# Kernel tuning notes

Hardware: AMD Instinct MI355X
Metric: run time of the kernel (lower is better)

Reference implementation:

```python
import math
import jax, jax.numpy as jnp
import numpy as np

N = 262144
DIMS_IN = 8
DIMS_C = 4
UNITS = 64
BINS = 10
N_PERMS = 3  # ceil(log2(8))
N_BLOCKS = 2 * N_PERMS
MIN_BW = 0.001
MIN_BH = 0.001
MIN_D = 0.001
EPS = 1e-6
LOG2 = float(np.log(2.0))


def build_masks():
    bits = np.array([[int(ch) for ch in np.binary_repr(i, N_PERMS)] for i in range(DIMS_IN)])
    bits = bits[:, ::-1].T  # (N_PERMS, DIMS_IN), LSB-first
    m = np.repeat(bits, 2, axis=0).astype(bool)  # repeat_interleave(2, dim=0)
    m[1::2] ^= True
    return m

MASKS = build_masks()  # (6, 8) bool, each row has 4 True


def rational_quadratic_spline(inputs, uw, uh, ud):
    # inputs: (N, D); uw/uh: (N, D, K); ud: (N, D, K+1). left=bottom=0, right=top=1.
    K = uw.shape[-1]
    widths = MIN_BW + (1.0 - MIN_BW * K) * jax.nn.softmax(uw, axis=-1)
    cw = jnp.cumsum(widths, axis=-1)
    cw = jnp.concatenate([jnp.zeros_like(cw[..., :1]), cw], axis=-1)
    cw = cw.at[..., -1].set(1.0)
    widths = cw[..., 1:] - cw[..., :-1]

    deriv = (MIN_D + jax.nn.softplus(ud)) / (MIN_D + LOG2)

    heights = MIN_BH + (1.0 - MIN_BH * K) * jax.nn.softmax(uh, axis=-1)
    ch = jnp.cumsum(heights, axis=-1)
    ch = jnp.concatenate([jnp.zeros_like(ch[..., :1]), ch], axis=-1)
    ch = ch.at[..., -1].set(1.0)
    heights = ch[..., 1:] - ch[..., :-1]

    # searchsorted on bin edges (forward uses cumwidths)
    locs = cw.at[..., -1].add(EPS)
    bin_idx = jnp.clip(jnp.sum(inputs[..., None] >= locs, axis=-1) - 1, 0, K - 1)
    g = lambda a: jnp.take_along_axis(a, bin_idx[..., None], axis=-1)[..., 0]

    in_cw = g(cw)
    in_bw = g(widths)
    in_ch = g(ch)
    delta = heights / widths
    in_delta = g(delta)
    in_d = g(deriv)
    in_dp1 = g(deriv[..., 1:])
    in_h = g(heights)

    theta = (inputs - in_cw) / in_bw
    tomt = theta * (1.0 - theta)
    numerator = in_h * (in_delta * theta ** 2 + in_d * tomt)
    denominator = in_delta + (in_d + in_dp1 - 2.0 * in_delta) * tomt
    outputs = in_ch + numerator / denominator
    deriv_num = in_delta ** 2 * (in_dp1 * theta ** 2 + 2.0 * in_delta * tomt + in_d * (1.0 - theta) ** 2)
    logabsdet = jnp.log(deriv_num) - 2.0 * jnp.log(denominator)
    return outputs, logabsdet


def unconstrained_rqs(inputs, uw, uh, ud):
    inside = jnp.all((inputs >= 0.0) & (inputs <= 1.0), axis=-1)  # (N,)
    x_in = jnp.clip(inputs, 0.0, 1.0)
    o, lad = rational_quadratic_spline(x_in, uw, uh, ud)
    outputs = jnp.where(inside[:, None], o, inputs)
    logabsdet = jnp.where(inside[:, None], lad, 0.0)
    return outputs, logabsdet


def setup_inputs() -> dict:
    key = jax.random.key(0)
    ks = jax.random.split(key, 10)
    out_dim = 4 * (3 * BINS + 1)  # every mask has 4 transformed dims
    in_dim = 4 + DIMS_C
    inp = {
        'x': jax.random.uniform(ks[0], (N, DIMS_IN), dtype=jnp.float32),
        'c': jax.random.normal(ks[1], (N, DIMS_C), dtype=jnp.float32),
        'W1': jax.random.normal(ks[2], (N_BLOCKS, in_dim, UNITS), dtype=jnp.float32) * 0.1,
        'b1': jax.random.normal(ks[3], (N_BLOCKS, UNITS), dtype=jnp.float32) * 0.1,
        'W2': jax.random.normal(ks[4], (N_BLOCKS, UNITS, UNITS), dtype=jnp.float32) * 0.1,
        'b2': jax.random.normal(ks[5], (N_BLOCKS, UNITS), dtype=jnp.float32) * 0.1,
        'W3': jax.random.normal(ks[6], (N_BLOCKS, UNITS, out_dim), dtype=jnp.float32) * 0.1,
        'b3': jax.random.normal(ks[7], (N_BLOCKS, out_dim), dtype=jnp.float32) * 0.1,
    }
    return inp


def reference(x, c, W1, b1, W2, b2, W3, b3):
    # ConditionalFlow.log_prob: forward transform, returns jac
    jac = jnp.zeros((x.shape[0],), dtype=x.dtype)
    for i in range(N_BLOCKS):
        mask = MASKS[i]
        cond_idx = np.nonzero(mask)[0]
        trafo_idx = np.nonzero(~mask)[0]
        x_cond = jnp.concatenate([x[:, cond_idx], c], axis=1)
        h = jax.nn.leaky_relu(x_cond @ W1[i] + b1[i], 0.01)
        h = jax.nn.leaky_relu(h @ W2[i] + b2[i], 0.01)
        out = (h @ W3[i] + b3[i]).reshape(x.shape[0], len(trafo_idx), 3 * BINS + 1)
        x_t = x[:, trafo_idx]
        x_out, bj = unconstrained_rqs(x_t, out[..., :BINS], out[..., BINS:2 * BINS], out[..., 2 * BINS:])
        x = x.at[:, trafo_idx].set(x_out)
        jac = jac + bj.sum(axis=1)
    return jac
```

## Files before the change

### kernel.cpp

```cpp
#include <hip/hip_runtime.h>
#include <hip/hip_bf16.h>
#include <math.h>

#define TPB 1024
#define NWV 16
#define WGS 256
#define NBLK 6
#define DNORM (1.0f / (0.001f + 0.69314718055994530942f))

typedef float  f32x4  __attribute__((ext_vector_type(4)));
typedef short  bf16x8 __attribute__((ext_vector_type(8)));

#define MFMA16(A, B, C) __builtin_amdgcn_mfma_f32_16x16x32_bf16((A), (B), (C), 0, 0, 0)


__device__ __forceinline__ float leaky(float a) { return a >= 0.f ? a : 0.01f * a; }

__device__ __forceinline__ unsigned int bfbits(float f) {
    unsigned int u = __float_as_uint(f);
    return (u + 0x7fffu + ((u >> 16) & 1u)) >> 16;
}

__device__ __forceinline__ unsigned int pkcvt(float a, float b) {
    __hip_bfloat162 t = __float22bfloat162_rn(make_float2(a, b));
    union { __hip_bfloat162 b2; unsigned int u; } cv;
    cv.b2 = t;
    return cv.u;
}

__global__ void prep_kernel(const float* __restrict__ W1, const float* __restrict__ B1,
                            const float* __restrict__ W2, const float* __restrict__ B2,
                            const float* __restrict__ W3, const float* __restrict__ B3,
                            unsigned short* __restrict__ wsf)
{
    const int blk = blockIdx.x;
    const int tid = threadIdx.x;
    unsigned short* baseA = wsf + blk * 1024;
    unsigned short* baseB = wsf + 6144 + blk * 12288;
    const float* w1 = W1 + blk * 512;
    const float* w2 = W2 + blk * 4096;
    const float* w3 = W3 + blk * 7936;

    if (tid < 512) {
        const int tile = tid >> 7, u = (tid >> 3) & 15, i = tid & 7;
        baseA[tid] = (unsigned short)bfbits(w1[i * 64 + tile * 16 + u]);
    }
    float* bb = reinterpret_cast<float*>(baseA + 512);
    if (tid >= 512 && tid < 576)        bb[tid - 512]      = B1[blk * 64 + (tid - 512)];
    else if (tid >= 576 && tid < 640)   bb[tid - 512]      = B2[blk * 64 + (tid - 576)];
    else if (tid >= 640 && tid < 768) {
        const int j = tid - 640;
        bb[128 + j] = (j < 124) ? B3[blk * 124 + j] : 0.f;
    }

    for (int e = tid; e < 4096; e += 1024) {
        const int ks = e >> 11, tile = (e >> 9) & 3, lane = (e >> 3) & 63, i = e & 7;
        const int k = ks * 32 + (lane >> 4) * 8 + i, col = tile * 16 + (lane & 15);
        baseB[e] = (unsigned short)bfbits(w2[k * 64 + col]);
    }
    for (int e = tid; e < 8192; e += 1024) {
        const int ks = e >> 12, tile = (e >> 9) & 7, lane = (e >> 3) & 63, i = e & 7;
        const int k = ks * 32 + (lane >> 4) * 8 + i, col = tile * 16 + (lane & 15);
        const float f = (col < 124) ? w3[k * 124 + col] : 0.f;
        baseB[4096 + e] = (unsigned short)bfbits(f);
    }
}

__global__ __launch_bounds__(TPB, 4) void flow_kernel(
    const float* __restrict__ X, const float* __restrict__ C4,
    const unsigned short* __restrict__ WSF, float* __restrict__ JAC)
{
    __shared__ __align__(16) unsigned short s_w[6144];
    __shared__ __align__(16) unsigned char  s_u[126976];
    __shared__ __align__(16) float          s_x[2304];

    const int tid   = threadIdx.x;
    const int wv    = tid >> 6;
    const int ln    = tid & 63;
    const int col16 = ln & 15;
    const int g     = ln >> 4;
    const int srow  = wv * 16 + col16;
    const int wgBase = blockIdx.x * WGS;

    unsigned short* hh = reinterpret_cast<unsigned short*>(s_u + wv * 7936);
    float*          op = reinterpret_cast<float*>(s_u + wv * 7936);

    {
        const int s  = tid >> 2;
        const int d0 = (tid & 3) * 2;
        const float2 xv = reinterpret_cast<const float2*>(X)[(size_t)(wgBase + s) * 4 + (tid & 3)];
        s_x[s * 9 + d0]     = xv.x;
        s_x[s * 9 + d0 + 1] = xv.y;
    }
    const float4 cvv = reinterpret_cast<const float4*>(C4)[(size_t)wgBase + srow];

    if (wv < 12) {
        const int off = wv * 512;
        __builtin_amdgcn_global_load_lds(
            (const __attribute__((address_space(1))) unsigned int*)(WSF + off + ln * 8),
            (__attribute__((address_space(3))) unsigned int*)(&s_w[off]),
            16, 0, 0);
    }
    __syncthreads();

    const int fB = g * 4;
    float jacl = 0.f;

    #pragma unroll 1
    for (int blk = 0; blk < NBLK; ++blk) {
        const int wA = blk * 1024;
        const float* biasf = reinterpret_cast<const float*>(&s_w[wA + 512]);
        const unsigned short* wBg = WSF + 6144 + blk * 12288;

        const int p  = blk >> 1;
        const int cb = (blk & 1) ^ 1;
        const int tb = blk & 1;
        const int lm = (1 << p) - 1;

        float xcf[8];
        #pragma unroll
        for (int j = 0; j < 4; ++j) {
            const int cd = ((j >> p) << (p + 1)) | (cb << p) | (j & lm);
            xcf[j] = s_x[srow * 9 + cd];
        }
        xcf[4] = cvv.x; xcf[5] = cvv.y; xcf[6] = cvv.z; xcf[7] = cvv.w;

        union { unsigned int u[4]; bf16x8 v; } bxh;
        #pragma unroll
        for (int q = 0; q < 4; ++q)
            bxh.u[q] = (g == 0) ? pkcvt(xcf[2 * q], xcf[2 * q + 1]) : 0u;

        #pragma unroll
        for (int tile = 0; tile < 4; ++tile) {
            f32x4 a1 = *reinterpret_cast<const f32x4*>(&biasf[tile * 16 + fB]);
            const bf16x8 wh = *reinterpret_cast<const bf16x8*>(&s_w[wA + tile * 128 + col16 * 8]);
            a1 = MFMA16(wh, bxh.v, a1);
            uint2 pw;
            pw.x = pkcvt(leaky(a1[0]), leaky(a1[1]));
            pw.y = pkcvt(leaky(a1[2]), leaky(a1[3]));
            *reinterpret_cast<uint2*>(&hh[col16 * 72 + tile * 16 + fB]) = pw;
        }

        f32x4 acc2[4];
        #pragma unroll
        for (int tile = 0; tile < 4; ++tile)
            acc2[tile] = *reinterpret_cast<const f32x4*>(&biasf[64 + tile * 16 + fB]);
        #pragma unroll
        for (int ks = 0; ks < 2; ++ks) {
            const bf16x8 hf = *reinterpret_cast<const bf16x8*>(&hh[col16 * 72 + ks * 32 + g * 8]);
            #pragma unroll
            for (int tile = 0; tile < 4; ++tile) {
                const bf16x8 wh = *reinterpret_cast<const bf16x8*>(
                    wBg + (ks * 4 + tile) * 512 + ln * 8);
                acc2[tile] = MFMA16(wh, hf, acc2[tile]);
            }
        }
        #pragma unroll
        for (int tile = 0; tile < 4; ++tile) {
            uint2 pw;
            pw.x = pkcvt(leaky(acc2[tile][0]), leaky(acc2[tile][1]));
            pw.y = pkcvt(leaky(acc2[tile][2]), leaky(acc2[tile][3]));
            *reinterpret_cast<uint2*>(&hh[col16 * 72 + tile * 16 + fB]) = pw;
        }

        f32x4 acc3[8];
        #pragma unroll
        for (int tile = 0; tile < 8; ++tile)
            acc3[tile] = *reinterpret_cast<const f32x4*>(&biasf[128 + tile * 16 + fB]);
        #pragma unroll
        for (int ks = 0; ks < 2; ++ks) {
            const bf16x8 hf = *reinterpret_cast<const bf16x8*>(&hh[col16 * 72 + ks * 32 + g * 8]);
            #pragma unroll
            for (int tile = 0; tile < 8; ++tile) {
                const bf16x8 wh = *reinterpret_cast<const bf16x8*>(
                    wBg + 4096 + (ks * 8 + tile) * 512 + ln * 8);
                acc3[tile] = MFMA16(wh, hf, acc3[tile]);
            }
        }

        #pragma unroll
        for (int tile = 0; tile < 8; ++tile)
            if (tile * 16 + fB < 124)
                *reinterpret_cast<f32x4*>(&op[col16 * 124 + tile * 16 + fB]) = acc3[tile];

        float xt[4];
        #pragma unroll
        for (int j = 0; j < 4; ++j) {
            const int td = ((j >> p) << (p + 1)) | (tb << p) | (j & lm);
            xt[j] = s_x[srow * 9 + td];
        }
        const float xmn = fminf(fminf(xt[0], xt[1]), fminf(xt[2], xt[3]));
        const float xmx = fmaxf(fmaxf(xt[0], xt[1]), fmaxf(xt[2], xt[3]));
        const bool inside = (xmn >= 0.f) && (xmx <= 1.f);
        float xtv = (g == 1) ? xt[1] : xt[0];
        xtv = (g == 2) ? xt[2] : xtv;
        xtv = (g == 3) ? xt[3] : xtv;
        const int ti = ((g >> p) << (p + 1)) | (tb << p) | (g & lm);

        float ov[31];
        {
            const float* ob = op + col16 * 124 + g * 31;
            #pragma unroll
            for (int j = 0; j < 31; ++j) ov[j] = ob[j];
        }

        float ew[10];
        #pragma unroll
        for (int k = 0; k < 10; ++k) ew[k] = __expf(ov[k]);
        const float sw = (((ew[0] + ew[1]) + (ew[2] + ew[3])) + ((ew[4] + ew[5]) + (ew[6] + ew[7])))
                         + (ew[8] + ew[9]);
        const float fw = 0.99f / sw;
        float Cw[11];
        Cw[0] = 0.f;
        #pragma unroll
        for (int k = 1; k <= 9; ++k) Cw[k] = Cw[k - 1] + (0.001f + ew[k - 1] * fw);
        Cw[10] = 1.0f;

        float eh[10];
        #pragma unroll
        for (int k = 0; k < 10; ++k) eh[k] = __expf(ov[10 + k]);
        const float sh = (((eh[0] + eh[1]) + (eh[2] + eh[3])) + ((eh[4] + eh[5]) + (eh[6] + eh[7])))
                         + (eh[8] + eh[9]);
        const float fh = 0.99f / sh;
        float Ch[11];
        Ch[0] = 0.f;
        #pragma unroll
        for (int k = 1; k <= 9; ++k) Ch[k] = Ch[k - 1] + (0.001f + eh[k - 1] * fh);
        Ch[10] = 1.0f;

        const float xin = fminf(fmaxf(xtv, 0.f), 1.f);
        float in_cw = 0.f, in_cwp1 = Cw[1], in_ch = 0.f, in_chp1 = Ch[1];
        float u_d = ov[20], u_dp1 = ov[21];
        #pragma unroll
        for (int k = 1; k < 10; ++k) {
            const bool ge = (xin >= Cw[k]);
            in_cw   = ge ? Cw[k]      : in_cw;
            in_cwp1 = ge ? Cw[k + 1]  : in_cwp1;
            in_ch   = ge ? Ch[k]      : in_ch;
            in_chp1 = ge ? Ch[k + 1]  : in_chp1;
            u_d     = ge ? ov[20 + k] : u_d;
            u_dp1   = ge ? ov[21 + k] : u_dp1;
        }
        const float in_bw = in_cwp1 - in_cw;
        const float in_h  = in_chp1 - in_ch;
        const float sp_d   = (u_d   > 15.f) ? u_d   : __logf(1.f + __expf(u_d));
        const float sp_dp1 = (u_dp1 > 15.f) ? u_dp1 : __logf(1.f + __expf(u_dp1));
        const float in_d   = (0.001f + sp_d)   * DNORM;
        const float in_dp1 = (0.001f + sp_dp1) * DNORM;

        const float th   = (xin - in_cw) / in_bw;
        const float tomt = th * (1.f - th);
        const float dl   = in_h / in_bw;
        const float nume = in_h * (dl * th * th + in_d * tomt);
        const float deno = dl + (in_d + in_dp1 - 2.f * dl) * tomt;
        const float xout = in_ch + nume / deno;
        const float omt  = 1.f - th;
        const float dnum = dl * dl * (in_dp1 * th * th + 2.f * dl * tomt + in_d * omt * omt);
        const float lad  = __logf(dnum) - 2.f * __logf(deno);

        jacl += inside ? lad : 0.f;
        s_x[srow * 9 + ti] = inside ? xout : xtv;
    }

    jacl += __shfl_xor(jacl, 16);
    jacl += __shfl_xor(jacl, 32);
    if (ln < 16)
        JAC[(size_t)wgBase + wv * 16 + ln] = jacl;
}

extern "C" void kernel_launch(void* const* d_in, const int* in_sizes, int n_in,
                              void* d_out, int out_size, void* d_ws, size_t ws_size,
                              hipStream_t stream) {
    (void)n_in; (void)ws_size;
    const float* X  = (const float*)d_in[0];
    const float* C4 = (const float*)d_in[1];
    const float* W1 = (const float*)d_in[2];
    const float* B1 = (const float*)d_in[3];
    const float* W2 = (const float*)d_in[4];
    const float* B2 = (const float*)d_in[5];
    const float* W3 = (const float*)d_in[6];
    const float* B3 = (const float*)d_in[7];
    float* out = (float*)d_out;
    unsigned short* wsf = (unsigned short*)d_ws;

    hipLaunchKernelGGL(prep_kernel, dim3(NBLK), dim3(1024), 0, stream,
                       W1, B1, W2, B2, W3, B3, wsf);

    const int n = in_sizes[0] / 8;
    hipLaunchKernelGGL(flow_kernel, dim3(n / WGS), dim3(TPB), 0, stream,
                       X, C4, wsf, out);
}
```

Measured before the change: 146.1 us.

## Shrink workgroups, keep x in registers, read weights from global, fold log2e into weights

Workgroups shrink from 1024 to 128 threads with a small per-wave LDS scratch. The LDS weight staging and the shared x buffer go away: x is held in registers and redistributed across lanes with shuffles, and weights and biases are read straight from global/L2. The block loop is fully unrolled, and LOG2E is folded into the softmax weight columns so native exp2/log2 can replace exp/log. The aim is higher occupancy and fewer barriers, at the cost of more global weight traffic and more register pressure.

```diff
diff --git a/kernel.cpp b/kernel.cpp
--- a/kernel.cpp
+++ b/kernel.cpp
@@ -2,16 +2,19 @@
 #include <hip/hip_bf16.h>
 #include <math.h>
 
-#define TPB 1024
-#define NWV 16
-#define WGS 256
+#define TPB 128
+#define WGS 32
 #define NBLK 6
 #define DNORM (1.0f / (0.001f + 0.69314718055994530942f))
+#define LOG2E 1.44269504088896340736f
+#define LN2   0.69314718055994530942f
 
 typedef float  f32x4  __attribute__((ext_vector_type(4)));
 typedef short  bf16x8 __attribute__((ext_vector_type(8)));
 
 #define MFMA16(A, B, C) __builtin_amdgcn_mfma_f32_16x16x32_bf16((A), (B), (C), 0, 0, 0)
+#define EXP2F(x) __builtin_amdgcn_exp2f(x)
+#define LOG2F(x) __builtin_amdgcn_logf(x)
 
 
 __device__ __forceinline__ float leaky(float a) { return a >= 0.f ? a : 0.01f * a; }
@@ -46,11 +49,16 @@
         baseA[tid] = (unsigned short)bfbits(w1[i * 64 + tile * 16 + u]);
     }
     float* bb = reinterpret_cast<float*>(baseA + 512);
-    if (tid >= 512 && tid < 576)        bb[tid - 512]      = B1[blk * 64 + (tid - 512)];
-    else if (tid >= 576 && tid < 640)   bb[tid - 512]      = B2[blk * 64 + (tid - 576)];
+    if (tid >= 512 && tid < 576)        bb[tid - 512] = B1[blk * 64 + (tid - 512)];
+    else if (tid >= 576 && tid < 640)   bb[tid - 512] = B2[blk * 64 + (tid - 576)];
     else if (tid >= 640 && tid < 768) {
         const int j = tid - 640;
-        bb[128 + j] = (j < 124) ? B3[blk * 124 + j] : 0.f;
+        float f = 0.f;
+        if (j < 124) {
+            f = B3[blk * 124 + j];
+            if (j % 31 < 20) f *= LOG2E;
+        }
+        bb[128 + j] = f;
     }
 
     for (int e = tid; e < 4096; e += 1024) {
@@ -61,67 +69,59 @@
     for (int e = tid; e < 8192; e += 1024) {
         const int ks = e >> 12, tile = (e >> 9) & 7, lane = (e >> 3) & 63, i = e & 7;
         const int k = ks * 32 + (lane >> 4) * 8 + i, col = tile * 16 + (lane & 15);
-        const float f = (col < 124) ? w3[k * 124 + col] : 0.f;
+        float f = 0.f;
+        if (col < 124) {
+            f = w3[k * 124 + col];
+            if (col % 31 < 20) f *= LOG2E;
+        }
         baseB[4096 + e] = (unsigned short)bfbits(f);
     }
 }
 
-__global__ __launch_bounds__(TPB, 4) void flow_kernel(
+__global__ __launch_bounds__(TPB, 5) void flow_kernel(
     const float* __restrict__ X, const float* __restrict__ C4,
     const unsigned short* __restrict__ WSF, float* __restrict__ JAC)
 {
-    __shared__ __align__(16) unsigned short s_w[6144];
-    __shared__ __align__(16) unsigned char  s_u[126976];
-    __shared__ __align__(16) float          s_x[2304];
+    __shared__ __align__(16) float s_o[2 * 1984];
 
     const int tid   = threadIdx.x;
     const int wv    = tid >> 6;
     const int ln    = tid & 63;
     const int col16 = ln & 15;
     const int g     = ln >> 4;
-    const int srow  = wv * 16 + col16;
-    const int wgBase = blockIdx.x * WGS;
-
-    unsigned short* hh = reinterpret_cast<unsigned short*>(s_u + wv * 7936);
-    float*          op = reinterpret_cast<float*>(s_u + wv * 7936);
-
-    {
-        const int s  = tid >> 2;
-        const int d0 = (tid & 3) * 2;
-        const float2 xv = reinterpret_cast<const float2*>(X)[(size_t)(wgBase + s) * 4 + (tid & 3)];
-        s_x[s * 9 + d0]     = xv.x;
-        s_x[s * 9 + d0 + 1] = xv.y;
-    }
-    const float4 cvv = reinterpret_cast<const float4*>(C4)[(size_t)wgBase + srow];
-
-    if (wv < 12) {
-        const int off = wv * 512;
-        __builtin_amdgcn_global_load_lds(
-            (const __attribute__((address_space(1))) unsigned int*)(WSF + off + ln * 8),
-            (__attribute__((address_space(3))) unsigned int*)(&s_w[off]),
-            16, 0, 0);
-    }
-    __syncthreads();
+    const size_t smp = (size_t)blockIdx.x * WGS + wv * 16 + col16;
+
+    float*          op = s_o + wv * 1984;
+    unsigned short* hh = reinterpret_cast<unsigned short*>(op);
+
+    const float4 xa = reinterpret_cast<const float4*>(X)[smp * 2 + 0];
+    const float4 xb = reinterpret_cast<const float4*>(X)[smp * 2 + 1];
+    float xr0 = xa.x, xr1 = xa.y, xr2 = xa.z, xr3 = xa.w;
+    float xr4 = xb.x, xr5 = xb.y, xr6 = xb.z, xr7 = xb.w;
+    const float4 cvv = reinterpret_cast<const float4*>(C4)[smp];
 
     const int fB = g * 4;
     float jacl = 0.f;
 
-    #pragma unroll 1
+    #pragma unroll
     for (int blk = 0; blk < NBLK; ++blk) {
-        const int wA = blk * 1024;
-        const float* biasf = reinterpret_cast<const float*>(&s_w[wA + 512]);
-        const unsigned short* wBg = WSF + 6144 + blk * 12288;
-
         const int p  = blk >> 1;
         const int cb = (blk & 1) ^ 1;
         const int tb = blk & 1;
         const int lm = (1 << p) - 1;
+        const unsigned short* wAg = WSF + blk * 1024;
+        const float* biasf = reinterpret_cast<const float*>(wAg + 512);
+        const unsigned short* wBg = WSF + 6144 + blk * 12288;
 
         float xcf[8];
         #pragma unroll
         for (int j = 0; j < 4; ++j) {
             const int cd = ((j >> p) << (p + 1)) | (cb << p) | (j & lm);
-            xcf[j] = s_x[srow * 9 + cd];
+            float v = xr0;
+            v = (cd == 1) ? xr1 : v; v = (cd == 2) ? xr2 : v; v = (cd == 3) ? xr3 : v;
+            v = (cd == 4) ? xr4 : v; v = (cd == 5) ? xr5 : v; v = (cd == 6) ? xr6 : v;
+            v = (cd == 7) ? xr7 : v;
+            xcf[j] = v;
         }
         xcf[4] = cvv.x; xcf[5] = cvv.y; xcf[6] = cvv.z; xcf[7] = cvv.w;
 
@@ -132,8 +132,8 @@
 
         #pragma unroll
         for (int tile = 0; tile < 4; ++tile) {
-            f32x4 a1 = *reinterpret_cast<const f32x4*>(&biasf[tile * 16 + fB]);
-            const bf16x8 wh = *reinterpret_cast<const bf16x8*>(&s_w[wA + tile * 128 + col16 * 8]);
+            f32x4 a1 = *reinterpret_cast<const f32x4*>(biasf + tile * 16 + fB);
+            const bf16x8 wh = *reinterpret_cast<const bf16x8*>(wAg + tile * 128 + col16 * 8);
             a1 = MFMA16(wh, bxh.v, a1);
             uint2 pw;
             pw.x = pkcvt(leaky(a1[0]), leaky(a1[1]));
@@ -144,7 +144,7 @@
         f32x4 acc2[4];
         #pragma unroll
         for (int tile = 0; tile < 4; ++tile)
-            acc2[tile] = *reinterpret_cast<const f32x4*>(&biasf[64 + tile * 16 + fB]);
+            acc2[tile] = *reinterpret_cast<const f32x4*>(biasf + 64 + tile * 16 + fB);
         #pragma unroll
         for (int ks = 0; ks < 2; ++ks) {
             const bf16x8 hf = *reinterpret_cast<const bf16x8*>(&hh[col16 * 72 + ks * 32 + g * 8]);
@@ -166,7 +166,7 @@
         f32x4 acc3[8];
         #pragma unroll
         for (int tile = 0; tile < 8; ++tile)
-            acc3[tile] = *reinterpret_cast<const f32x4*>(&biasf[128 + tile * 16 + fB]);
+            acc3[tile] = *reinterpret_cast<const f32x4*>(biasf + 128 + tile * 16 + fB);
         #pragma unroll
         for (int ks = 0; ks < 2; ++ks) {
             const bf16x8 hf = *reinterpret_cast<const bf16x8*>(&hh[col16 * 72 + ks * 32 + g * 8]);
@@ -187,7 +187,11 @@
         #pragma unroll
         for (int j = 0; j < 4; ++j) {
             const int td = ((j >> p) << (p + 1)) | (tb << p) | (j & lm);
-            xt[j] = s_x[srow * 9 + td];
+            float v = xr0;
+            v = (td == 1) ? xr1 : v; v = (td == 2) ? xr2 : v; v = (td == 3) ? xr3 : v;
+            v = (td == 4) ? xr4 : v; v = (td == 5) ? xr5 : v; v = (td == 6) ? xr6 : v;
+            v = (td == 7) ? xr7 : v;
+            xt[j] = v;
         }
         const float xmn = fminf(fminf(xt[0], xt[1]), fminf(xt[2], xt[3]));
         const float xmx = fmaxf(fmaxf(xt[0], xt[1]), fmaxf(xt[2], xt[3]));
@@ -195,7 +199,6 @@
         float xtv = (g == 1) ? xt[1] : xt[0];
         xtv = (g == 2) ? xt[2] : xtv;
         xtv = (g == 3) ? xt[3] : xtv;
-        const int ti = ((g >> p) << (p + 1)) | (tb << p) | (g & lm);
 
         float ov[31];
         {
@@ -206,7 +209,7 @@
 
         float ew[10];
         #pragma unroll
-        for (int k = 0; k < 10; ++k) ew[k] = __expf(ov[k]);
+        for (int k = 0; k < 10; ++k) ew[k] = EXP2F(ov[k]);
         const float sw = (((ew[0] + ew[1]) + (ew[2] + ew[3])) + ((ew[4] + ew[5]) + (ew[6] + ew[7])))
                          + (ew[8] + ew[9]);
         const float fw = 0.99f / sw;
@@ -218,7 +221,7 @@
 
         float eh[10];
         #pragma unroll
-        for (int k = 0; k < 10; ++k) eh[k] = __expf(ov[10 + k]);
+        for (int k = 0; k < 10; ++k) eh[k] = EXP2F(ov[10 + k]);
         const float sh = (((eh[0] + eh[1]) + (eh[2] + eh[3])) + ((eh[4] + eh[5]) + (eh[6] + eh[7])))
                          + (eh[8] + eh[9]);
         const float fh = 0.99f / sh;
@@ -256,16 +259,26 @@
         const float xout = in_ch + nume / deno;
         const float omt  = 1.f - th;
         const float dnum = dl * dl * (in_dp1 * th * th + 2.f * dl * tomt + in_d * omt * omt);
-        const float lad  = __logf(dnum) - 2.f * __logf(deno);
-
+        const float lad  = LN2 * (LOG2F(dnum) - 2.f * LOG2F(deno));
+
+        const float xnew = inside ? xout : xtv;
         jacl += inside ? lad : 0.f;
-        s_x[srow * 9 + ti] = inside ? xout : xtv;
+
+        #pragma unroll
+        for (int j = 0; j < 4; ++j) {
+            const int dj = ((j >> p) << (p + 1)) | (tb << p) | (j & lm);
+            const float v = __shfl(xnew, col16 + 16 * j, 64);
+            if (dj == 0) xr0 = v; else if (dj == 1) xr1 = v;
+            else if (dj == 2) xr2 = v; else if (dj == 3) xr3 = v;
+            else if (dj == 4) xr4 = v; else if (dj == 5) xr5 = v;
+            else if (dj == 6) xr6 = v; else xr7 = v;
+        }
     }
 
     jacl += __shfl_xor(jacl, 16);
     jacl += __shfl_xor(jacl, 32);
     if (ln < 16)
-        JAC[(size_t)wgBase + wv * 16 + ln] = jacl;
+        JAC[(size_t)blockIdx.x * WGS + wv * 16 + ln] = jacl;
 }
 
 extern "C" void kernel_launch(void* const* d_in, const int* in_sizes, int n_in,
```

Result: slower. 179.4 us (+22.8%).
